# Performance work log

Hardware: AMD Instinct MI355X
Metric: run time of the kernel (lower is better)

## Reference

```python
import jax, jax.numpy as jnp
import numpy as np

E = 2048   # embed_dim
H = 16     # num_heads
D = E // H # head_dim = 128
ROPE_BASE = 10000.0


def setup_inputs() -> dict:
    key = jax.random.key(0)
    ks = jax.random.split(key, 9)
    s = 0.02
    x = jax.random.normal(ks[0], (2, 2048, E), dtype=jnp.float32)
    Wq = jax.random.normal(ks[1], (E, E), dtype=jnp.float32) * s
    bq = jax.random.normal(ks[2], (E,), dtype=jnp.float32) * s
    Wk = jax.random.normal(ks[3], (E, E), dtype=jnp.float32) * s
    bk = jax.random.normal(ks[4], (E,), dtype=jnp.float32) * s
    Wv = jax.random.normal(ks[5], (E, E), dtype=jnp.float32) * s
    bv = jax.random.normal(ks[6], (E,), dtype=jnp.float32) * s
    Wo = jax.random.normal(ks[7], (E, E), dtype=jnp.float32) * s
    bo = jax.random.normal(ks[8], (E,), dtype=jnp.float32) * s
    return {"x": x, "Wq": Wq, "bq": bq, "Wk": Wk, "bk": bk,
            "Wv": Wv, "bv": bv, "Wo": Wo, "bo": bo}


def _rope_cos_sin(seq_len, dtype):
    inv_freq = 1.0 / (ROPE_BASE ** (jnp.arange(0, D, 2, dtype=jnp.float32) / D))
    pos = jnp.arange(seq_len, dtype=jnp.float32)
    freqs = pos[:, None] * inv_freq[None, :]          # (S, D/2)
    emb = jnp.concatenate([freqs, freqs], axis=-1)    # (S, D)
    return jnp.cos(emb).astype(dtype), jnp.sin(emb).astype(dtype)


def _rotate_half(t):
    t1, t2 = jnp.split(t, 2, axis=-1)
    return jnp.concatenate([-t2, t1], axis=-1)


def reference(x, Wq, bq, Wk, bk, Wv, bv, Wo, bo):
    B, S, _ = x.shape
    # QKV projections (torch Linear: x @ W.T + b)
    q = (x @ Wq.T + bq).reshape(B, S, H, D).transpose(0, 2, 1, 3)  # (B,H,S,D)
    k = (x @ Wk.T + bk).reshape(B, S, H, D).transpose(0, 2, 1, 3)
    v = (x @ Wv.T + bv).reshape(B, S, H, D).transpose(0, 2, 1, 3)
    # RoPE
    cos, sin = _rope_cos_sin(S, x.dtype)              # (S, D) each
    q = q * cos + _rotate_half(q) * sin
    k = k * cos + _rotate_half(k) * sin
    # Causal scaled dot-product attention
    scale = 1.0 / jnp.sqrt(jnp.asarray(D, dtype=x.dtype))
    scores = jnp.einsum('bhqd,bhkd->bhqk', q, k) * scale
    causal = jnp.tril(jnp.ones((S, S), dtype=bool))
    scores = jnp.where(causal, scores, jnp.asarray(-jnp.inf, dtype=x.dtype))
    attn = jax.nn.softmax(scores, axis=-1)
    out = jnp.einsum('bhqk,bhkd->bhqd', attn, v)      # (B,H,S,D)
    out = out.transpose(0, 2, 1, 3).reshape(B, S, E)
    return out @ Wo.T + bo
```

## Files before the change

### kernel.cpp

```cpp
#include <hip/hip_runtime.h>
#include <math.h>

typedef __bf16 bf16;
typedef __attribute__((ext_vector_type(2))) __bf16 bf16x2;
typedef __attribute__((ext_vector_type(4))) __bf16 bf16x4;
typedef __attribute__((ext_vector_type(8))) __bf16 bf16x8;
typedef __attribute__((ext_vector_type(4))) float f32x4;

#define GLD16(g, l) __builtin_amdgcn_global_load_lds( \
    (const __attribute__((address_space(1))) void*)(g), \
    (__attribute__((address_space(3))) void*)(l), 16, 0, 0)

template<int N> __device__ __forceinline__ void wait_vm() {
  static_assert(N == 0 || N == 2 || N == 3 || N == 4, "");
  if constexpr (N == 0) asm volatile("s_waitcnt vmcnt(0)" ::: "memory");
  else if constexpr (N == 2) asm volatile("s_waitcnt vmcnt(2)" ::: "memory");
  else if constexpr (N == 3) asm volatile("s_waitcnt vmcnt(3)" ::: "memory");
  else asm volatile("s_waitcnt vmcnt(4)" ::: "memory");
}

__global__ void prep_kernel(const float* __restrict__ x,
                            const float* __restrict__ Wq, const float* __restrict__ Wk,
                            const float* __restrict__ Wv, const float* __restrict__ Wo,
                            const float* __restrict__ bq, const float* __restrict__ bk,
                            const float* __restrict__ bv,
                            bf16* __restrict__ xb, bf16* __restrict__ wqkv, bf16* __restrict__ wob,
                            float* __restrict__ biasq, float* __restrict__ cost, float* __restrict__ sint) {
  const int bid = blockIdx.x, t = threadIdx.x;
  if (bid < 24576) {
    const float* src;
    bf16* dst;
    int i;
    if (bid < 8192)       { src = x;  dst = xb;                    i = bid * 256 + t; }
    else if (bid < 12288) { src = Wq; dst = wqkv;                  i = (bid - 8192) * 256 + t; }
    else if (bid < 16384) { src = Wk; dst = wqkv + 2048 * 2048;    i = (bid - 12288) * 256 + t; }
    else if (bid < 20480) { src = Wv; dst = wqkv + 2 * 2048 * 2048; i = (bid - 16384) * 256 + t; }
    else                  { src = Wo; dst = wob;                   i = (bid - 20480) * 256 + t; }
    float4 f = ((const float4*)src)[i];
    bf16x4 o;
    o[0] = (bf16)f.x; o[1] = (bf16)f.y; o[2] = (bf16)f.z; o[3] = (bf16)f.w;
    ((bf16x4*)dst)[i] = o;
  } else if (bid < 25088) {
    int i = (bid - 24576) * 256 + t;
    int s = i >> 6, d = i & 63;
    float inv = powf(10000.0f, -(float)d / 64.0f);
    float ang = (float)s * inv;
    cost[i] = cosf(ang);
    sint[i] = sinf(ang);
  } else {
    int i = (bid - 25088) * 256 + t;
    biasq[i] = (i < 2048) ? bq[i] : (i < 4096 ? bk[i - 2048] : bv[i - 4096]);
  }
}

__global__ void rope_k_kernel(const bf16* __restrict__ qkv,
                              const float* __restrict__ cost, const float* __restrict__ sint,
                              bf16* __restrict__ kr) {
  int idx = blockIdx.x * blockDim.x + threadIdx.x;
  int dp = idx & 15;
  int h = (idx >> 4) & 15;
  int s = (idx >> 8) & 2047;
  int b = idx >> 19;
  int d0 = dp * 4;
  const bf16* row = qkv + ((size_t)(b * 2048 + s) * 6144) + 2048 + h * 128;
  bf16x4 klo = *(const bf16x4*)&row[d0];
  bf16x4 khi = *(const bf16x4*)&row[d0 + 64];
  float4 c4 = *(const float4*)&cost[(s << 6) + d0];
  float4 s4 = *(const float4*)&sint[(s << 6) + d0];
  float cf[4] = {c4.x, c4.y, c4.z, c4.w};
  float sf[4] = {s4.x, s4.y, s4.z, s4.w};
  bf16x4 olo, ohi;
#pragma unroll
  for (int j = 0; j < 4; ++j) {
    float kl = (float)klo[j], kh = (float)khi[j];
    olo[j] = (bf16)(kl * cf[j] - kh * sf[j]);
    ohi[j] = (bf16)(kh * cf[j] + kl * sf[j]);
  }
  bf16* orow = kr + (((size_t)(b * 16 + h) * 2048 + s) * 128);
  *(bf16x4*)&orow[d0] = olo;
  *(bf16x4*)&orow[d0 + 64] = ohi;
}

__global__ void transpose_v_kernel(const bf16* __restrict__ qkv, bf16* __restrict__ vt) {
  __shared__ bf16 Vl[64 * 72];
  const int bh = blockIdx.z;
  const int st = blockIdx.y;
  const int dt = blockIdx.x;
  const int b = bh >> 4, h = bh & 15;
  const bf16* src = qkv + ((size_t)(b * 2048 + st * 64) * 6144) + 4096 + h * 128 + dt * 64;
  bf16* dst = vt + ((size_t)bh * 128 + dt * 64) * 2048 + st * 64;
  const int t = threadIdx.x;
#pragma unroll
  for (int i = 0; i < 2; ++i) {
    int c = i * 256 + t;
    int r = c >> 3, c0 = (c & 7) * 8;
    *(bf16x8*)&Vl[r * 72 + c0] = *(const bf16x8*)&src[(size_t)r * 6144 + c0];
  }
  __syncthreads();
#pragma unroll
  for (int i = 0; i < 2; ++i) {
    int c = i * 256 + t;
    int r = c >> 3, c0 = (c & 7) * 8;
    bf16x8 v;
#pragma unroll
    for (int j = 0; j < 8; ++j) v[j] = Vl[(c0 + j) * 72 + r];
    *(bf16x8*)&dst[(size_t)r * 2048 + c0] = v;
  }
}

template<int BN, bool OUT_BF16, int LOGNX>
__global__ __launch_bounds__(512, 2)
void gemm256_kernel(const bf16* __restrict__ A, const bf16* __restrict__ B,
                    const float* __restrict__ bias, void* __restrict__ Cp,
                    int M, int N, int K) {
  constexpr int NB = BN / 64;
  __shared__ bf16 Al[2][2][128 * 64];
  __shared__ bf16 Bl[2][NB][64 * 64];
  const int t = threadIdx.x;
  const int wid = t >> 6, lane = t & 63;
  const int wr = wid >> 2, wc = wid & 3;
  const int lr = lane & 15, lk = lane >> 4;
  const int nwg = (int)(gridDim.x * gridDim.y);
  const int flat = (int)(blockIdx.y * gridDim.x + blockIdx.x);
  const int fs = (flat & 7) * (nwg >> 3) + (flat >> 3);
  const int tn = fs & ((1 << LOGNX) - 1);
  const int tm = fs >> LOGNX;
  const bf16* Ab = A + (size_t)tm * 256 * K;
  const bf16* Bb = B + (size_t)tn * BN * K;
  const int NT = K >> 6;

  auto stageA = [&](int bp, int h, int kt) {
#pragma unroll
    for (int q = 0; q < 2; ++q) {
      int e = q * 512 + t;
      int r = e >> 3, c = e & 7;
      GLD16(Ab + (size_t)(h * 128 + r) * K + kt * 64 + ((c ^ (r & 7)) << 3), &Al[bp][h][e * 8]);
    }
  };
  auto stageB = [&](int bp, int unit, int kt) {
    int r = t >> 3, c = t & 7;
    GLD16(Bb + (size_t)(unit * 64 + r) * K + kt * 64 + ((c ^ (r & 7)) << 3), &Bl[bp][unit][t * 8]);
  };

  f32x4 acc[8][NB] = {};

#pragma unroll
  for (int un = 0; un < NB; ++un) stageB(0, un, 0);
  stageA(0, 0, 0); stageA(0, 1, 0);
  if (NT > 1) {
#pragma unroll
    for (int un = 0; un < NB; ++un) stageB(1, un, 1);
    wait_vm<NB>();
  } else {
    wait_vm<0>();
  }
  __builtin_amdgcn_s_barrier();
  __builtin_amdgcn_sched_barrier(0);

  for (int u = 0; u < NT; ++u) {
    const int p = u & 1;
    const bf16* Ah = Al[p][wr];
    bf16x8 bfr[NB][2];
#pragma unroll
    for (int j = 0; j < 4; ++j) {
      bf16x8 afr[2][2];
      if (j == 0) {
#pragma unroll
        for (int n = 0; n < NB; ++n)
#pragma unroll
          for (int kk = 0; kk < 2; ++kk) {
            int rb = wc * (NB * 16) + n * 16 + lr;
            bfr[n][kk] = *(const bf16x8*)&Bl[p][rb >> 6][(rb & 63) * 64 + ((((kk << 2) | lk) ^ (rb & 7)) << 3)];
          }
      }
#pragma unroll
      for (int m2 = 0; m2 < 2; ++m2)
#pragma unroll
        for (int kk = 0; kk < 2; ++kk) {
          int r = (2 * j + m2) * 16 + lr;
          afr[m2][kk] = *(const bf16x8*)&Ah[r * 64 + ((((kk << 2) | lk) ^ (r & 7)) << 3)];
        }
      if (j == 0)      { if (u + 1 < NT) stageA(p ^ 1, 0, u + 1); }
      else if (j == 1) { if (u + 1 < NT) stageA(p ^ 1, 1, u + 1); }
      else if (j == 2) {
        if (u + 2 < NT) {
#pragma unroll
          for (int un = 0; un < NB / 2; ++un) stageB(p, un, u + 2);
        }
      } else {
        if (u + 2 < NT) {
#pragma unroll
          for (int un = NB / 2; un < NB; ++un) stageB(p, un, u + 2);
        }
      }
      __builtin_amdgcn_s_barrier();
      asm volatile("s_waitcnt lgkmcnt(0)" ::: "memory");
      __builtin_amdgcn_sched_barrier(0);
      __builtin_amdgcn_s_setprio(1);
#pragma unroll
      for (int m2 = 0; m2 < 2; ++m2)
#pragma unroll
        for (int n = 0; n < NB; ++n)
#pragma unroll
          for (int kk = 0; kk < 2; ++kk)
            acc[2 * j + m2][n] = __builtin_amdgcn_mfma_f32_16x16x32_bf16(
                afr[m2][kk], bfr[n][kk], acc[2 * j + m2][n], 0, 0, 0);
      __builtin_amdgcn_s_setprio(0);
      __builtin_amdgcn_sched_barrier(0);
      if (j == 3) {
        if (u + 2 < NT) { wait_vm<NB>(); }
        else            { wait_vm<0>(); }
      }
      __builtin_amdgcn_s_barrier();
      __builtin_amdgcn_sched_barrier(0);
    }
  }

  const int rb = tm * 256 + wr * 128, cb = tn * BN + wc * (NB * 16);
#pragma unroll
  for (int n = 0; n < NB; ++n) {
    int col = cb + n * 16 + lr;
    float bvl = bias[col];
#pragma unroll
    for (int m = 0; m < 8; ++m) {
#pragma unroll
      for (int r = 0; r < 4; ++r) {
        int row = rb + m * 16 + lk * 4 + r;
        float v = acc[m][n][r] + bvl;
        if (OUT_BF16) ((bf16*)Cp)[(size_t)row * N + col] = (bf16)v;
        else          ((float*)Cp)[(size_t)row * N + col] = v;
      }
    }
  }
}

__global__ __launch_bounds__(256, 2)
void attn_kernel(const bf16* __restrict__ qkv, const bf16* __restrict__ Kc,
                 const bf16* __restrict__ Vtg, const float* __restrict__ cost,
                 const float* __restrict__ sint, bf16* __restrict__ O, int S) {
  __shared__ bf16 Kl[2][64 * 128];
  __shared__ bf16 Vt[2][128 * 64];
  __shared__ bf16 Pl[4][16 * 64];
  const int t = threadIdx.x, wid = t >> 6, lane = t & 63;
  const int lr = lane & 15, lk = lane >> 4;
  const int bh = blockIdx.y;
  const int b = bh >> 4, h = bh & 15;
  const int NQ = S >> 6;
  const int qtA = blockIdx.x, qtB = NQ - 1 - qtA;
  const int ntA = qtA + 1, ntB = qtB + 1, total = ntA + ntB;
  const bf16* Kb = Kc + (size_t)bh * S * 128;
  const bf16* Vb = Vtg + (size_t)bh * 128 * S;
  const float scale = 0.08838834764831845f;

  bf16x8 qf[4];
  auto loadQ = [&](int q0) {
    int qrow = q0 + wid * 16 + lr;
    const bf16* qp = qkv + (size_t)(b * 2048 + qrow) * 6144 + h * 128;
    bf16x8 raw[4];
#pragma unroll
    for (int kb = 0; kb < 4; ++kb) raw[kb] = *(const bf16x8*)&qp[kb * 32 + lk * 8];
#pragma unroll
    for (int kb = 0; kb < 4; ++kb) {
      const float* cb = cost + (qrow << 6) + ((kb & 1) << 5) + lk * 8;
      const float* sb = sint + (qrow << 6) + ((kb & 1) << 5) + lk * 8;
#pragma unroll
      for (int j = 0; j < 8; ++j) {
        float qv = (float)raw[kb][j];
        float qo = (float)raw[kb ^ 2][j];
        float rot = (kb < 2) ? -qo : qo;
        qf[kb][j] = (bf16)(qv * cb[j] + rot * sb[j]);
      }
    }
  };
  auto stage = [&](int buf, int kv0) {
#pragma unroll
    for (int c = 0; c < 4; ++c) {
      int fc = c * 256 + t;
      int kvr = fc >> 4, cc = fc & 15;
      GLD16(Kb + (size_t)(kv0 + kvr) * 128 + (cc ^ (kvr & 7)) * 8, &Kl[buf][fc * 8]);
      int dr = fc >> 3, c2 = fc & 7;
      GLD16(Vb + (size_t)dr * S + kv0 + (c2 ^ (dr & 7)) * 8, &Vt[buf][fc * 8]);
    }
  };

  f32x4 o[8] = {};
  float mrun[4], lrun[4];
#pragma unroll
  for (int r = 0; r < 4; ++r) { mrun[r] = -INFINITY; lrun[r] = 0.f; }

  loadQ(qtA * 64);
  stage(0, 0);
  __syncthreads();
  int cur = 0;
  for (int ti = 0; ti < total; ++ti) {
    if (ti + 1 < total) {
      int tn = ti + 1;
      stage(cur ^ 1, ((tn < ntA) ? tn : tn - ntA) * 64);
    }
    __builtin_amdgcn_sched_barrier(0);
    const bool isA = ti < ntA;
    const int tt = isA ? ti : ti - ntA;
    const int nt = isA ? ntA : ntB;
    const int q0 = (isA ? qtA : qtB) * 64;
    const int kv0 = tt * 64;
    f32x4 sa[4];
    __builtin_amdgcn_s_setprio(1);
#pragma unroll
    for (int n = 0; n < 4; ++n) {
      sa[n] = (f32x4){0.f, 0.f, 0.f, 0.f};
      int kvl = n * 16 + lr;
#pragma unroll
      for (int kb = 0; kb < 4; ++kb) {
        bf16x8 kf = *(const bf16x8*)&Kl[cur][kvl * 128 + (((kb << 2) | lk) ^ (kvl & 7)) * 8];
        sa[n] = __builtin_amdgcn_mfma_f32_16x16x32_bf16(qf[kb], kf, sa[n], 0, 0, 0);
      }
    }
    __builtin_amdgcn_s_setprio(0);
    float p[4][4];
    float tmax[4] = {-INFINITY, -INFINITY, -INFINITY, -INFINITY};
    const bool lastTile = (tt == nt - 1);
#pragma unroll
    for (int n = 0; n < 4; ++n)
#pragma unroll
      for (int r = 0; r < 4; ++r) {
        float s = sa[n][r] * scale;
        if (lastTile) {
          int kvg = kv0 + n * 16 + lr;
          int qg = q0 + wid * 16 + lk * 4 + r;
          if (kvg > qg) s = -INFINITY;
        }
        p[n][r] = s;
        tmax[r] = fmaxf(tmax[r], s);
      }
#pragma unroll
    for (int r = 0; r < 4; ++r)
#pragma unroll
      for (int off = 1; off < 16; off <<= 1)
        tmax[r] = fmaxf(tmax[r], __shfl_xor(tmax[r], off));
    float alpha[4], rsum[4];
#pragma unroll
    for (int r = 0; r < 4; ++r) {
      float mnew = fmaxf(mrun[r], tmax[r]);
      alpha[r] = __expf(mrun[r] - mnew);
      mrun[r] = mnew;
      rsum[r] = 0.f;
#pragma unroll
      for (int n = 0; n < 4; ++n) {
        p[n][r] = __expf(p[n][r] - mnew);
        rsum[r] += p[n][r];
      }
    }
#pragma unroll
    for (int r = 0; r < 4; ++r) {
#pragma unroll
      for (int off = 1; off < 16; off <<= 1)
        rsum[r] += __shfl_xor(rsum[r], off);
      lrun[r] = lrun[r] * alpha[r] + rsum[r];
    }
#pragma unroll
    for (int n8 = 0; n8 < 8; ++n8)
#pragma unroll
      for (int r = 0; r < 4; ++r)
        o[n8][r] *= alpha[r];
#pragma unroll
    for (int n = 0; n < 4; ++n)
#pragma unroll
      for (int r = 0; r < 4; ++r) {
        int row = lk * 4 + r, col = n * 16 + lr;
        Pl[wid][(row * 64 + col) ^ ((row & 7) << 3)] = (bf16)p[n][r];
      }
    __builtin_amdgcn_s_setprio(1);
#pragma unroll
    for (int kb2 = 0; kb2 < 2; ++kb2) {
      bf16x8 pf = *(const bf16x8*)&Pl[wid][(lr * 64 + kb2 * 32 + lk * 8) ^ ((lr & 7) << 3)];
#pragma unroll
      for (int n8 = 0; n8 < 8; ++n8) {
        int dcol = n8 * 16 + lr;
        bf16x8 vf = *(const bf16x8*)&Vt[cur][(dcol * 64 + kb2 * 32 + lk * 8) ^ ((dcol & 7) << 3)];
        o[n8] = __builtin_amdgcn_mfma_f32_16x16x32_bf16(pf, vf, o[n8], 0, 0, 0);
      }
    }
    __builtin_amdgcn_s_setprio(0);
    if (ti == ntA - 1) {
#pragma unroll
      for (int r = 0; r < 4; ++r) {
        float rl = 1.0f / lrun[r];
        int row = qtA * 64 + wid * 16 + lk * 4 + r;
        size_t base = ((size_t)(b * S + row)) * 2048 + h * 128;
#pragma unroll
        for (int n8 = 0; n8 < 8; ++n8)
          O[base + n8 * 16 + lr] = (bf16)(o[n8][r] * rl);
      }
#pragma unroll
      for (int n8 = 0; n8 < 8; ++n8) o[n8] = (f32x4){0.f, 0.f, 0.f, 0.f};
#pragma unroll
      for (int r = 0; r < 4; ++r) { mrun[r] = -INFINITY; lrun[r] = 0.f; }
      loadQ(qtB * 64);
    }
    __syncthreads();
    cur ^= 1;
  }
#pragma unroll
  for (int r = 0; r < 4; ++r) {
    float rl = 1.0f / lrun[r];
    int row = qtB * 64 + wid * 16 + lk * 4 + r;
    size_t base = ((size_t)(b * S + row)) * 2048 + h * 128;
#pragma unroll
    for (int n8 = 0; n8 < 8; ++n8)
      O[base + n8 * 16 + lr] = (bf16)(o[n8][r] * rl);
  }
}


extern "C" void kernel_launch(void* const* d_in, const int* in_sizes, int n_in,
                              void* d_out, int out_size, void* d_ws, size_t ws_size,
                              hipStream_t stream) {
  const float* x  = (const float*)d_in[0];
  const float* Wq = (const float*)d_in[1];
  const float* bq = (const float*)d_in[2];
  const float* Wk = (const float*)d_in[3];
  const float* bk = (const float*)d_in[4];
  const float* Wv = (const float*)d_in[5];
  const float* bv = (const float*)d_in[6];
  const float* Wo = (const float*)d_in[7];
  const float* bo = (const float*)d_in[8];

  char* ws = (char*)d_ws;
  bf16* xb     = (bf16*)(ws);
  bf16* wqkv   = (bf16*)(ws + 16777216);
  bf16* wob    = (bf16*)(ws + 41943040);
  bf16* qkv    = (bf16*)(ws + 50331648);
  bf16* kr     = (bf16*)(ws + 100663296);
  bf16* vt     = (bf16*)(ws + 117440512);
  float* biasq = (float*)(ws + 134217728);
  float* cost  = (float*)(ws + 134242304);
  float* sint  = (float*)(ws + 134766592);
  bf16* attn_out = xb;

  prep_kernel<<<25112, 256, 0, stream>>>(x, Wq, Wk, Wv, Wo, bq, bk, bv,
                                         xb, wqkv, wob, biasq, cost, sint);
  gemm256_kernel<192, true, 5><<<dim3(32, 16), 512, 0, stream>>>(xb, wqkv, biasq, qkv, 4096, 6144, 2048);
  rope_k_kernel<<<4096, 256, 0, stream>>>(qkv, cost, sint, kr);
  transpose_v_kernel<<<dim3(2, 32, 32), 256, 0, stream>>>(qkv, vt);
  attn_kernel<<<dim3(16, 32), 256, 0, stream>>>(qkv, kr, vt, cost, sint, attn_out, 2048);
  gemm256_kernel<128, false, 4><<<dim3(16, 16), 512, 0, stream>>>(attn_out, wob, bo, (float*)d_out, 4096, 2048, 2048);
}
```

Measured before the change: 299.2 us.

## Triple-buffer GEMM A tiles with two-ahead prefetch; merge RoPE-K and V-transpose kernels

The GEMM kernel gains a third LDS buffer for A tiles, so A is now prefetched two k-steps ahead like B, and the vmcnt waits are widened to match the extra loads in flight. B staging for all units moves into one sub-step, with A staging split over the next two. Separately, the RoPE-on-K and V-transpose kernels become one launch that branches on block index, saving a kernel launch. The extra A buffer raises LDS use per block (now about 144-160KB for two blocks), which may threaten the two-blocks-per-CU occupancy set by the launch bounds.

```diff
diff --git a/kernel.cpp b/kernel.cpp
--- a/kernel.cpp
+++ b/kernel.cpp
@@ -12,11 +12,10 @@
     (__attribute__((address_space(3))) void*)(l), 16, 0, 0)
 
 template<int N> __device__ __forceinline__ void wait_vm() {
-  static_assert(N == 0 || N == 2 || N == 3 || N == 4, "");
+  static_assert(N == 0 || N == 6 || N == 7, "");
   if constexpr (N == 0) asm volatile("s_waitcnt vmcnt(0)" ::: "memory");
-  else if constexpr (N == 2) asm volatile("s_waitcnt vmcnt(2)" ::: "memory");
-  else if constexpr (N == 3) asm volatile("s_waitcnt vmcnt(3)" ::: "memory");
-  else asm volatile("s_waitcnt vmcnt(4)" ::: "memory");
+  else if constexpr (N == 6) asm volatile("s_waitcnt vmcnt(6)" ::: "memory");
+  else asm volatile("s_waitcnt vmcnt(7)" ::: "memory");
 }
 
 __global__ void prep_kernel(const float* __restrict__ x,
@@ -53,58 +52,57 @@
   }
 }
 
-__global__ void rope_k_kernel(const bf16* __restrict__ qkv,
-                              const float* __restrict__ cost, const float* __restrict__ sint,
-                              bf16* __restrict__ kr) {
-  int idx = blockIdx.x * blockDim.x + threadIdx.x;
-  int dp = idx & 15;
-  int h = (idx >> 4) & 15;
-  int s = (idx >> 8) & 2047;
-  int b = idx >> 19;
-  int d0 = dp * 4;
-  const bf16* row = qkv + ((size_t)(b * 2048 + s) * 6144) + 2048 + h * 128;
-  bf16x4 klo = *(const bf16x4*)&row[d0];
-  bf16x4 khi = *(const bf16x4*)&row[d0 + 64];
-  float4 c4 = *(const float4*)&cost[(s << 6) + d0];
-  float4 s4 = *(const float4*)&sint[(s << 6) + d0];
-  float cf[4] = {c4.x, c4.y, c4.z, c4.w};
-  float sf[4] = {s4.x, s4.y, s4.z, s4.w};
-  bf16x4 olo, ohi;
-#pragma unroll
-  for (int j = 0; j < 4; ++j) {
-    float kl = (float)klo[j], kh = (float)khi[j];
-    olo[j] = (bf16)(kl * cf[j] - kh * sf[j]);
-    ohi[j] = (bf16)(kh * cf[j] + kl * sf[j]);
-  }
-  bf16* orow = kr + (((size_t)(b * 16 + h) * 2048 + s) * 128);
-  *(bf16x4*)&orow[d0] = olo;
-  *(bf16x4*)&orow[d0 + 64] = ohi;
-}
-
-__global__ void transpose_v_kernel(const bf16* __restrict__ qkv, bf16* __restrict__ vt) {
+__global__ void rope_tv_kernel(const bf16* __restrict__ qkv,
+                               const float* __restrict__ cost, const float* __restrict__ sint,
+                               bf16* __restrict__ kr, bf16* __restrict__ vt) {
   __shared__ bf16 Vl[64 * 72];
-  const int bh = blockIdx.z;
-  const int st = blockIdx.y;
-  const int dt = blockIdx.x;
-  const int b = bh >> 4, h = bh & 15;
-  const bf16* src = qkv + ((size_t)(b * 2048 + st * 64) * 6144) + 4096 + h * 128 + dt * 64;
-  bf16* dst = vt + ((size_t)bh * 128 + dt * 64) * 2048 + st * 64;
   const int t = threadIdx.x;
-#pragma unroll
-  for (int i = 0; i < 2; ++i) {
-    int c = i * 256 + t;
-    int r = c >> 3, c0 = (c & 7) * 8;
-    *(bf16x8*)&Vl[r * 72 + c0] = *(const bf16x8*)&src[(size_t)r * 6144 + c0];
-  }
-  __syncthreads();
-#pragma unroll
-  for (int i = 0; i < 2; ++i) {
-    int c = i * 256 + t;
-    int r = c >> 3, c0 = (c & 7) * 8;
-    bf16x8 v;
-#pragma unroll
-    for (int j = 0; j < 8; ++j) v[j] = Vl[(c0 + j) * 72 + r];
-    *(bf16x8*)&dst[(size_t)r * 2048 + c0] = v;
+  if (blockIdx.x < 4096) {
+    int idx = blockIdx.x * 256 + t;
+    int dp = idx & 15;
+    int h = (idx >> 4) & 15;
+    int s = (idx >> 8) & 2047;
+    int b = idx >> 19;
+    int d0 = dp * 4;
+    const bf16* row = qkv + ((size_t)(b * 2048 + s) * 6144) + 2048 + h * 128;
+    bf16x4 klo = *(const bf16x4*)&row[d0];
+    bf16x4 khi = *(const bf16x4*)&row[d0 + 64];
+    float4 c4 = *(const float4*)&cost[(s << 6) + d0];
+    float4 s4 = *(const float4*)&sint[(s << 6) + d0];
+    float cf[4] = {c4.x, c4.y, c4.z, c4.w};
+    float sf[4] = {s4.x, s4.y, s4.z, s4.w};
+    bf16x4 olo, ohi;
+#pragma unroll
+    for (int j = 0; j < 4; ++j) {
+      float kl = (float)klo[j], kh = (float)khi[j];
+      olo[j] = (bf16)(kl * cf[j] - kh * sf[j]);
+      ohi[j] = (bf16)(kh * cf[j] + kl * sf[j]);
+    }
+    bf16* orow = kr + (((size_t)(b * 16 + h) * 2048 + s) * 128);
+    *(bf16x4*)&orow[d0] = olo;
+    *(bf16x4*)&orow[d0 + 64] = ohi;
+  } else {
+    int vbid = blockIdx.x - 4096;
+    const int dt = vbid & 1, st = (vbid >> 1) & 31, bh = vbid >> 6;
+    const int b = bh >> 4, h = bh & 15;
+    const bf16* src = qkv + ((size_t)(b * 2048 + st * 64) * 6144) + 4096 + h * 128 + dt * 64;
+    bf16* dst = vt + ((size_t)bh * 128 + dt * 64) * 2048 + st * 64;
+#pragma unroll
+    for (int i = 0; i < 2; ++i) {
+      int c = i * 256 + t;
+      int r = c >> 3, c0 = (c & 7) * 8;
+      *(bf16x8*)&Vl[r * 72 + c0] = *(const bf16x8*)&src[(size_t)r * 6144 + c0];
+    }
+    __syncthreads();
+#pragma unroll
+    for (int i = 0; i < 2; ++i) {
+      int c = i * 256 + t;
+      int r = c >> 3, c0 = (c & 7) * 8;
+      bf16x8 v;
+#pragma unroll
+      for (int j = 0; j < 8; ++j) v[j] = Vl[(c0 + j) * 72 + r];
+      *(bf16x8*)&dst[(size_t)r * 2048 + c0] = v;
+    }
   }
 }
 
@@ -114,7 +112,7 @@
                     const float* __restrict__ bias, void* __restrict__ Cp,
                     int M, int N, int K) {
   constexpr int NB = BN / 64;
-  __shared__ bf16 Al[2][2][128 * 64];
+  __shared__ bf16 Al[3][2][128 * 64];
   __shared__ bf16 Bl[2][NB][64 * 64];
   const int t = threadIdx.x;
   const int wid = t >> 6, lane = t & 63;
@@ -129,12 +127,12 @@
   const bf16* Bb = B + (size_t)tn * BN * K;
   const int NT = K >> 6;
 
-  auto stageA = [&](int bp, int h, int kt) {
+  auto stageA = [&](int slot, int h, int kt) {
 #pragma unroll
     for (int q = 0; q < 2; ++q) {
       int e = q * 512 + t;
       int r = e >> 3, c = e & 7;
-      GLD16(Ab + (size_t)(h * 128 + r) * K + kt * 64 + ((c ^ (r & 7)) << 3), &Al[bp][h][e * 8]);
+      GLD16(Ab + (size_t)(h * 128 + r) * K + kt * 64 + ((c ^ (r & 7)) << 3), &Al[slot][h][e * 8]);
     }
   };
   auto stageB = [&](int bp, int unit, int kt) {
@@ -150,7 +148,8 @@
   if (NT > 1) {
 #pragma unroll
     for (int un = 0; un < NB; ++un) stageB(1, un, 1);
-    wait_vm<NB>();
+    stageA(1, 0, 1); stageA(1, 1, 1);
+    wait_vm<NB + 4>();
   } else {
     wait_vm<0>();
   }
@@ -159,7 +158,9 @@
 
   for (int u = 0; u < NT; ++u) {
     const int p = u & 1;
-    const bf16* Ah = Al[p][wr];
+    const int as = u % 3;
+    const int s2 = (u + 2) % 3;
+    const bf16* Ah = Al[as][wr];
     bf16x8 bfr[NB][2];
 #pragma unroll
     for (int j = 0; j < 4; ++j) {
@@ -180,19 +181,13 @@
           int r = (2 * j + m2) * 16 + lr;
           afr[m2][kk] = *(const bf16x8*)&Ah[r * 64 + ((((kk << 2) | lk) ^ (r & 7)) << 3)];
         }
-      if (j == 0)      { if (u + 1 < NT) stageA(p ^ 1, 0, u + 1); }
-      else if (j == 1) { if (u + 1 < NT) stageA(p ^ 1, 1, u + 1); }
-      else if (j == 2) {
+      if (j == 1) {
         if (u + 2 < NT) {
 #pragma unroll
-          for (int un = 0; un < NB / 2; ++un) stageB(p, un, u + 2);
+          for (int un = 0; un < NB; ++un) stageB(p, un, u + 2);
         }
-      } else {
-        if (u + 2 < NT) {
-#pragma unroll
-          for (int un = NB / 2; un < NB; ++un) stageB(p, un, u + 2);
-        }
-      }
+      } else if (j == 2) { if (u + 2 < NT) stageA(s2, 0, u + 2); }
+      else if (j == 3)   { if (u + 2 < NT) stageA(s2, 1, u + 2); }
       __builtin_amdgcn_s_barrier();
       asm volatile("s_waitcnt lgkmcnt(0)" ::: "memory");
       __builtin_amdgcn_sched_barrier(0);
@@ -208,7 +203,7 @@
       __builtin_amdgcn_s_setprio(0);
       __builtin_amdgcn_sched_barrier(0);
       if (j == 3) {
-        if (u + 2 < NT) { wait_vm<NB>(); }
+        if (u + 2 < NT) { wait_vm<NB + 4>(); }
         else            { wait_vm<0>(); }
       }
       __builtin_amdgcn_s_barrier();
@@ -440,8 +435,7 @@
   prep_kernel<<<25112, 256, 0, stream>>>(x, Wq, Wk, Wv, Wo, bq, bk, bv,
                                          xb, wqkv, wob, biasq, cost, sint);
   gemm256_kernel<192, true, 5><<<dim3(32, 16), 512, 0, stream>>>(xb, wqkv, biasq, qkv, 4096, 6144, 2048);
-  rope_k_kernel<<<4096, 256, 0, stream>>>(qkv, cost, sint, kr);
-  transpose_v_kernel<<<dim3(2, 32, 32), 256, 0, stream>>>(qkv, vt);
+  rope_tv_kernel<<<6144, 256, 0, stream>>>(qkv, cost, sint, kr, vt);
   attn_kernel<<<dim3(16, 32), 256, 0, stream>>>(qkv, kr, vt, cost, sint, attn_out, 2048);
   gemm256_kernel<128, false, 4><<<dim3(16, 16), 512, 0, stream>>>(attn_out, wob, bo, (float*)d_out, 4096, 2048, 2048);
 }
```

Result: slower. 314.4 us (+5.1%).

## Remap workgroups to XCDs for L2 locality and fuse RoPE-K with V transpose

Applied to the files above, without the earlier changes.

Replaces the GEMM tile swizzle with an explicit XCD-aware mapping, so workgroups landing on the same XCD (flat & 7) share A row-tiles and their operands stay in that XCD's L2. The attention grid is flattened the same way, so each XCD handles a fixed group of four heads whose K/V stay local. The separate RoPE-K and V-transpose kernels are merged into one launch to save a kernel launch and gap. The new mapping hardcodes tile counts (16 M tiles, fixed head grouping), which ties it to these shapes.

```diff
diff --git a/kernel.cpp b/kernel.cpp
--- a/kernel.cpp
+++ b/kernel.cpp
@@ -12,11 +12,10 @@
     (__attribute__((address_space(3))) void*)(l), 16, 0, 0)
 
 template<int N> __device__ __forceinline__ void wait_vm() {
-  static_assert(N == 0 || N == 2 || N == 3 || N == 4, "");
+  static_assert(N == 0 || N == 2 || N == 3, "");
   if constexpr (N == 0) asm volatile("s_waitcnt vmcnt(0)" ::: "memory");
   else if constexpr (N == 2) asm volatile("s_waitcnt vmcnt(2)" ::: "memory");
-  else if constexpr (N == 3) asm volatile("s_waitcnt vmcnt(3)" ::: "memory");
-  else asm volatile("s_waitcnt vmcnt(4)" ::: "memory");
+  else asm volatile("s_waitcnt vmcnt(3)" ::: "memory");
 }
 
 __global__ void prep_kernel(const float* __restrict__ x,
@@ -53,62 +52,61 @@
   }
 }
 
-__global__ void rope_k_kernel(const bf16* __restrict__ qkv,
-                              const float* __restrict__ cost, const float* __restrict__ sint,
-                              bf16* __restrict__ kr) {
-  int idx = blockIdx.x * blockDim.x + threadIdx.x;
-  int dp = idx & 15;
-  int h = (idx >> 4) & 15;
-  int s = (idx >> 8) & 2047;
-  int b = idx >> 19;
-  int d0 = dp * 4;
-  const bf16* row = qkv + ((size_t)(b * 2048 + s) * 6144) + 2048 + h * 128;
-  bf16x4 klo = *(const bf16x4*)&row[d0];
-  bf16x4 khi = *(const bf16x4*)&row[d0 + 64];
-  float4 c4 = *(const float4*)&cost[(s << 6) + d0];
-  float4 s4 = *(const float4*)&sint[(s << 6) + d0];
-  float cf[4] = {c4.x, c4.y, c4.z, c4.w};
-  float sf[4] = {s4.x, s4.y, s4.z, s4.w};
-  bf16x4 olo, ohi;
-#pragma unroll
-  for (int j = 0; j < 4; ++j) {
-    float kl = (float)klo[j], kh = (float)khi[j];
-    olo[j] = (bf16)(kl * cf[j] - kh * sf[j]);
-    ohi[j] = (bf16)(kh * cf[j] + kl * sf[j]);
-  }
-  bf16* orow = kr + (((size_t)(b * 16 + h) * 2048 + s) * 128);
-  *(bf16x4*)&orow[d0] = olo;
-  *(bf16x4*)&orow[d0 + 64] = ohi;
-}
-
-__global__ void transpose_v_kernel(const bf16* __restrict__ qkv, bf16* __restrict__ vt) {
+__global__ void rope_tv_kernel(const bf16* __restrict__ qkv,
+                               const float* __restrict__ cost, const float* __restrict__ sint,
+                               bf16* __restrict__ kr, bf16* __restrict__ vt) {
   __shared__ bf16 Vl[64 * 72];
-  const int bh = blockIdx.z;
-  const int st = blockIdx.y;
-  const int dt = blockIdx.x;
-  const int b = bh >> 4, h = bh & 15;
-  const bf16* src = qkv + ((size_t)(b * 2048 + st * 64) * 6144) + 4096 + h * 128 + dt * 64;
-  bf16* dst = vt + ((size_t)bh * 128 + dt * 64) * 2048 + st * 64;
   const int t = threadIdx.x;
-#pragma unroll
-  for (int i = 0; i < 2; ++i) {
-    int c = i * 256 + t;
-    int r = c >> 3, c0 = (c & 7) * 8;
-    *(bf16x8*)&Vl[r * 72 + c0] = *(const bf16x8*)&src[(size_t)r * 6144 + c0];
-  }
-  __syncthreads();
-#pragma unroll
-  for (int i = 0; i < 2; ++i) {
-    int c = i * 256 + t;
-    int r = c >> 3, c0 = (c & 7) * 8;
-    bf16x8 v;
-#pragma unroll
-    for (int j = 0; j < 8; ++j) v[j] = Vl[(c0 + j) * 72 + r];
-    *(bf16x8*)&dst[(size_t)r * 2048 + c0] = v;
-  }
-}
-
-template<int BN, bool OUT_BF16, int LOGNX>
+  if (blockIdx.x < 4096) {
+    int idx = blockIdx.x * 256 + t;
+    int dp = idx & 15;
+    int h = (idx >> 4) & 15;
+    int s = (idx >> 8) & 2047;
+    int b = idx >> 19;
+    int d0 = dp * 4;
+    const bf16* row = qkv + ((size_t)(b * 2048 + s) * 6144) + 2048 + h * 128;
+    bf16x4 klo = *(const bf16x4*)&row[d0];
+    bf16x4 khi = *(const bf16x4*)&row[d0 + 64];
+    float4 c4 = *(const float4*)&cost[(s << 6) + d0];
+    float4 s4 = *(const float4*)&sint[(s << 6) + d0];
+    float cf[4] = {c4.x, c4.y, c4.z, c4.w};
+    float sf[4] = {s4.x, s4.y, s4.z, s4.w};
+    bf16x4 olo, ohi;
+#pragma unroll
+    for (int j = 0; j < 4; ++j) {
+      float kl = (float)klo[j], kh = (float)khi[j];
+      olo[j] = (bf16)(kl * cf[j] - kh * sf[j]);
+      ohi[j] = (bf16)(kh * cf[j] + kl * sf[j]);
+    }
+    bf16* orow = kr + (((size_t)(b * 16 + h) * 2048 + s) * 128);
+    *(bf16x4*)&orow[d0] = olo;
+    *(bf16x4*)&orow[d0 + 64] = ohi;
+  } else {
+    int vbid = blockIdx.x - 4096;
+    const int dt = vbid & 1, st = (vbid >> 1) & 31, bh = vbid >> 6;
+    const int b = bh >> 4, h = bh & 15;
+    const bf16* src = qkv + ((size_t)(b * 2048 + st * 64) * 6144) + 4096 + h * 128 + dt * 64;
+    bf16* dst = vt + ((size_t)bh * 128 + dt * 64) * 2048 + st * 64;
+#pragma unroll
+    for (int i = 0; i < 2; ++i) {
+      int c = i * 256 + t;
+      int r = c >> 3, c0 = (c & 7) * 8;
+      *(bf16x8*)&Vl[r * 72 + c0] = *(const bf16x8*)&src[(size_t)r * 6144 + c0];
+    }
+    __syncthreads();
+#pragma unroll
+    for (int i = 0; i < 2; ++i) {
+      int c = i * 256 + t;
+      int r = c >> 3, c0 = (c & 7) * 8;
+      bf16x8 v;
+#pragma unroll
+      for (int j = 0; j < 8; ++j) v[j] = Vl[(c0 + j) * 72 + r];
+      *(bf16x8*)&dst[(size_t)r * 2048 + c0] = v;
+    }
+  }
+}
+
+template<int BN, bool OUT_BF16>
 __global__ __launch_bounds__(512, 2)
 void gemm256_kernel(const bf16* __restrict__ A, const bf16* __restrict__ B,
                     const float* __restrict__ bias, void* __restrict__ Cp,
@@ -120,11 +118,10 @@
   const int wid = t >> 6, lane = t & 63;
   const int wr = wid >> 2, wc = wid & 3;
   const int lr = lane & 15, lk = lane >> 4;
-  const int nwg = (int)(gridDim.x * gridDim.y);
-  const int flat = (int)(blockIdx.y * gridDim.x + blockIdx.x);
-  const int fs = (flat & 7) * (nwg >> 3) + (flat >> 3);
-  const int tn = fs & ((1 << LOGNX) - 1);
-  const int tm = fs >> LOGNX;
+  const int flat = (int)blockIdx.x;
+  const int xcd = flat & 7, kb2 = flat >> 3;
+  const int tm = xcd * 2 + (kb2 & 1);
+  const int tn = kb2 >> 1;
   const bf16* Ab = A + (size_t)tm * 256 * K;
   const bf16* Bb = B + (size_t)tn * BN * K;
   const int NT = K >> 6;
@@ -243,10 +240,12 @@
   __shared__ bf16 Pl[4][16 * 64];
   const int t = threadIdx.x, wid = t >> 6, lane = t & 63;
   const int lr = lane & 15, lk = lane >> 4;
-  const int bh = blockIdx.y;
+  const int flat = (int)blockIdx.x;
+  const int xcd = flat & 7, kk2 = flat >> 3;
+  const int bh = xcd * 4 + (kk2 >> 4);
   const int b = bh >> 4, h = bh & 15;
   const int NQ = S >> 6;
-  const int qtA = blockIdx.x, qtB = NQ - 1 - qtA;
+  const int qtA = kk2 & 15, qtB = NQ - 1 - qtA;
   const int ntA = qtA + 1, ntB = qtB + 1, total = ntA + ntB;
   const bf16* Kb = Kc + (size_t)bh * S * 128;
   const bf16* Vb = Vtg + (size_t)bh * 128 * S;
@@ -439,9 +438,8 @@
 
   prep_kernel<<<25112, 256, 0, stream>>>(x, Wq, Wk, Wv, Wo, bq, bk, bv,
                                          xb, wqkv, wob, biasq, cost, sint);
-  gemm256_kernel<192, true, 5><<<dim3(32, 16), 512, 0, stream>>>(xb, wqkv, biasq, qkv, 4096, 6144, 2048);
-  rope_k_kernel<<<4096, 256, 0, stream>>>(qkv, cost, sint, kr);
-  transpose_v_kernel<<<dim3(2, 32, 32), 256, 0, stream>>>(qkv, vt);
-  attn_kernel<<<dim3(16, 32), 256, 0, stream>>>(qkv, kr, vt, cost, sint, attn_out, 2048);
-  gemm256_kernel<128, false, 4><<<dim3(16, 16), 512, 0, stream>>>(attn_out, wob, bo, (float*)d_out, 4096, 2048, 2048);
-}
+  gemm256_kernel<192, true><<<512, 512, 0, stream>>>(xb, wqkv, biasq, qkv, 4096, 6144, 2048);
+  rope_tv_kernel<<<6144, 256, 0, stream>>>(qkv, cost, sint, kr, vt);
+  attn_kernel<<<512, 256, 0, stream>>>(qkv, kr, vt, cost, sint, attn_out, 2048);
+  gemm256_kernel<128, false><<<256, 512, 0, stream>>>(attn_out, wob, bo, (float*)d_out, 4096, 2048, 2048);
+}
```

Measured after the change: 289.5 us. 1.03x faster.
